# Kernel tuning notes

Hardware: AMD Instinct MI355X
Metric: run time of the kernel (lower is better)

Reference implementation:

```python
import jax, jax.numpy as jnp
import numpy as np

EPS = 1e-5
NHEAD = 8

def layer_norm(x, g, b):
    mu = jnp.mean(x, axis=-1, keepdims=True)
    var = jnp.mean((x - mu) ** 2, axis=-1, keepdims=True)
    return (x - mu) * jax.lax.rsqrt(var + EPS) * g + b

def setup_inputs() -> dict:
    key = jax.random.key(0)
    ks = jax.random.split(key, 8)
    B, S, D, F = 4, 2048, 512, 2048
    s = 0.02
    return {
        "x": jax.random.normal(ks[0], (B, S, D), jnp.float32),
        "Wqkv": jax.random.normal(ks[1], (3 * D, D), jnp.float32) * s,
        "bqkv": jnp.zeros((3 * D,), jnp.float32),
        "Wo": jax.random.normal(ks[2], (D, D), jnp.float32) * s,
        "bo": jnp.zeros((D,), jnp.float32),
        "W1": jax.random.normal(ks[3], (F, D), jnp.float32) * s,
        "b1": jnp.zeros((F,), jnp.float32),
        "W2": jax.random.normal(ks[4], (D, F), jnp.float32) * s,
        "b2": jnp.zeros((D,), jnp.float32),
        "g1": jnp.ones((D,), jnp.float32),
        "bn1": jnp.zeros((D,), jnp.float32),
        "g2": jnp.ones((D,), jnp.float32),
        "bn2": jnp.zeros((D,), jnp.float32),
    }

def reference(x, Wqkv, bqkv, Wo, bo, W1, b1, W2, b2, g1, bn1, g2, bn2):
    B, S, D = x.shape
    H = NHEAD
    hd = D // H
    # fused QKV projection (torch MultiheadAttention in_proj)
    qkv = x @ Wqkv.T + bqkv                      # [B,S,3D]
    q, k, v = jnp.split(qkv, 3, axis=-1)
    q = q.reshape(B, S, H, hd).transpose(0, 2, 1, 3)  # [B,H,S,hd]
    k = k.reshape(B, S, H, hd).transpose(0, 2, 1, 3)
    v = v.reshape(B, S, H, hd).transpose(0, 2, 1, 3)
    scores = jnp.einsum("bhqd,bhkd->bhqk", q, k) / jnp.sqrt(jnp.float32(hd))
    causal = jnp.tril(jnp.ones((S, S), bool))
    scores = jnp.where(causal, scores, jnp.float32(-jnp.inf))
    attn = jax.nn.softmax(scores, axis=-1)
    ctx = jnp.einsum("bhqk,bhkd->bhqd", attn, v)        # [B,H,S,hd]
    ctx = ctx.transpose(0, 2, 1, 3).reshape(B, S, D)
    attn_out = ctx @ Wo.T + bo
    # residual + LayerNorm 1
    x = layer_norm(x + attn_out, g1, bn1)
    # FFN (ReLU) + residual + LayerNorm 2
    ff = jax.nn.relu(x @ W1.T + b1) @ W2.T + b2
    x = layer_norm(x + ff, g2, bn2)
    return x
```

## Files before the change

kernel.cpp:

```cpp
#include <hip/hip_runtime.h>
#include <hip/hip_bf16.h>
#include <math.h>

#define D_MODEL 512
#define SEQ     2048
#define BATCH   4
#define NHEADS  8
#define HDIM    64
#define FFN     2048
#define TOKENS  (BATCH*SEQ)

typedef __attribute__((ext_vector_type(8))) short bf16x8;
typedef __attribute__((ext_vector_type(4))) float f32x4;
typedef __attribute__((ext_vector_type(4))) unsigned u32x4;

__device__ inline ushort f2bf(float f) {
    unsigned u = __builtin_bit_cast(unsigned, f);
    unsigned r = (u + 0x7fffu + ((u >> 16) & 1u)) >> 16;
    return (ushort)r;
}

#define GLOAD_LDS16(g, l) __builtin_amdgcn_global_load_lds( \
    (const __attribute__((address_space(1))) void*)(g), \
    (__attribute__((address_space(3))) void*)(l), 16, 0, 0)

__global__ void cast_all_bf16(const float* __restrict__ x, const float* __restrict__ Wqkv,
                              const float* __restrict__ Wo, const float* __restrict__ W1,
                              const float* __restrict__ W2, ushort* __restrict__ outbase) {
    const int i = blockIdx.x * blockDim.x + threadIdx.x;
    if (i >= 1835008) return;
    float4 v;
    if      (i < 1048576) v = ((const float4*)x)[i];
    else if (i < 1245184) v = ((const float4*)Wqkv)[i - 1048576];
    else if (i < 1310720) v = ((const float4*)Wo)[i - 1245184];
    else if (i < 1572864) v = ((const float4*)W1)[i - 1310720];
    else                  v = ((const float4*)W2)[i - 1572864];
    ushort4 o;
    o.x = f2bf(v.x); o.y = f2bf(v.y); o.z = f2bf(v.z); o.w = f2bf(v.w);
    ((ushort4*)outbase)[i] = o;
}

template<int MODE, int RELU, int BM, int BN>
__global__ __launch_bounds__(BN == 256 ? 512 : 256)
void gemm_bt_mfma(const ushort* __restrict__ A,
                  const ushort* __restrict__ W,
                  const float* __restrict__ bias,
                  void* __restrict__ CoutA,
                  ushort* __restrict__ Qc,
                  ushort* __restrict__ Kc,
                  ushort* __restrict__ Vt,
                  int M, int N, int Kstride, int Klen) {
    constexpr int NW    = (BN == 256) ? 8 : 4;
    constexpr int WC    = NW / 2;
    constexpr int MI    = BM / 32;
    constexpr int AROWS = BM / NW;
    constexpr bool A2   = (AROWS == 32);
    __shared__ ushort Asb[3][BM * 32];
    __shared__ ushort Bsb[3][BN * 32];

    const int tid  = threadIdx.x;
    const int lane = tid & 63;
    const int wv   = tid >> 6;

    const int Gx = gridDim.x;
    const int f  = blockIdx.x + Gx * blockIdx.y;
    const int xc = f & 7;
    const int j  = f >> 3;
    const int ni = j % Gx;
    const int mi = xc * (gridDim.y >> 3) + j / Gx;
    const int m0 = mi * BM;
    const int n0 = ni * BN;

    const int wm = (wv / WC) * (BM / 2);
    const int wn = (wv % WC) * 64;

    const int rA = wv * AROWS + (lane >> 2);
    const int rB = wv * 32 + (lane >> 2);
    const int cS = (((lane & 3) ^ ((lane >> 3) & 3)) * 8);
    const ushort* gA0 = A + (size_t)(m0 + rA) * Kstride + cS;
    const ushort* gA1 = gA0 + (size_t)16 * Kstride;
    const ushort* gB0 = W + (size_t)(n0 + rB) * Kstride + cS;
    const ushort* gB1 = gB0 + (size_t)16 * Kstride;

    f32x4 acc[MI][4] = {};

    const int fr  = lane & 15;
    const int fks = (((lane >> 4) ^ ((fr >> 1) & 3)) * 8);
    const int loA = wv * (AROWS * 32);
    const int loB = wv * 1024;

#define STAGE(ab, bb) do { \
        GLOAD_LDS16(gA0, (ab) + loA); \
        if constexpr (A2) GLOAD_LDS16(gA1, (ab) + loA + 512); \
        GLOAD_LDS16(gB0, (bb) + loB); \
        GLOAD_LDS16(gB1, (bb) + loB + 512); \
        gA0 += 32; if constexpr (A2) gA1 += 32; \
        gB0 += 32; gB1 += 32; } while (0)

#define COMPUTE(ab, bb) do { \
        bf16x8 af_[MI], bf_[4]; \
        _Pragma("unroll") \
        for (int i_ = 0; i_ < MI; ++i_) \
            af_[i_] = *(const bf16x8*)((ab) + (wm + i_ * 16 + fr) * 32 + fks); \
        _Pragma("unroll") \
        for (int j_ = 0; j_ < 4; ++j_) \
            bf_[j_] = *(const bf16x8*)((bb) + (wn + j_ * 16 + fr) * 32 + fks); \
        _Pragma("unroll") \
        for (int i_ = 0; i_ < MI; ++i_) \
            _Pragma("unroll") \
            for (int j_ = 0; j_ < 4; ++j_) \
                acc[i_][j_] = __builtin_amdgcn_mfma_f32_16x16x32_bf16(af_[i_], bf_[j_], acc[i_][j_], 0, 0, 0); \
        } while (0)

#define PWAIT do { \
        if constexpr (A2) asm volatile("s_waitcnt vmcnt(4)" ::: "memory"); \
        else              asm volatile("s_waitcnt vmcnt(3)" ::: "memory"); \
        __builtin_amdgcn_s_barrier(); \
        __builtin_amdgcn_sched_barrier(0); } while (0)

    ushort *Ac = Asb[0], *An = Asb[1], *As = Asb[2];
    ushort *Bc = Bsb[0], *Bn = Bsb[1], *Bs = Bsb[2];

    STAGE(Ac, Bc);
    STAGE(An, Bn);
    const int ntiles = Klen >> 5;
    for (int t = 0; t < ntiles - 1; ++t) {
        PWAIT;
        if (t + 2 < ntiles) STAGE(As, Bs);
        COMPUTE(Ac, Bc);
        ushort* tA = Ac; Ac = An; An = As; As = tA;
        ushort* tB = Bc; Bc = Bn; Bn = Bs; Bs = tB;
    }
    asm volatile("s_waitcnt vmcnt(0)" ::: "memory");
    __builtin_amdgcn_s_barrier();
    __builtin_amdgcn_sched_barrier(0);
    COMPUTE(Ac, Bc);

#undef STAGE
#undef COMPUTE
#undef PWAIT

    const int col  = lane & 15;
    const int rowq = (lane >> 4) * 4;
    #pragma unroll
    for (int i = 0; i < MI; ++i) {
        const int gm = m0 + wm + i * 16 + rowq;
        #pragma unroll
        for (int j2 = 0; j2 < 4; ++j2) {
            const int gn = n0 + wn + j2 * 16 + col;
            if (MODE == 2) {
                const float bv = bias[gn];
                const int seg = gn >> 9;
                const int h   = (gn >> 6) & 7;
                const int dd  = gn & 63;
                const int bb  = gm >> 11;
                const int ss  = gm & 2047;
                const int bh  = bb * 8 + h;
                if (seg == 2) {
                    ushort4 pk;
                    pk.x = f2bf(acc[i][j2][0] + bv);
                    pk.y = f2bf(acc[i][j2][1] + bv);
                    pk.z = f2bf(acc[i][j2][2] + bv);
                    pk.w = f2bf(acc[i][j2][3] + bv);
                    *(ushort4*)(Vt + ((size_t)bh * 64 + dd) * 2048 + ss) = pk;
                } else {
                    ushort* dst = (seg == 0 ? Qc : Kc) + ((size_t)bh * 2048 + ss) * 64 + dd;
                    #pragma unroll
                    for (int r = 0; r < 4; ++r)
                        dst[(size_t)r * 64] = f2bf(acc[i][j2][r] + bv);
                }
            } else if (MODE == 3) {
                float* dst = (float*)CoutA;
                const float bv = bias[gn];
                #pragma unroll
                for (int r = 0; r < 4; ++r)
                    dst[(size_t)(gm + r) * N + gn] = acc[i][j2][r] + bv;
            } else {
                const float bv = bias[gn];
                #pragma unroll
                for (int r = 0; r < 4; ++r) {
                    float v = acc[i][j2][r] + bv;
                    if (RELU) v = fmaxf(v, 0.f);
                    ((ushort*)CoutA)[(size_t)(gm + r) * N + gn] = f2bf(v);
                }
            }
        }
    }
}

__device__ __forceinline__ void attn_step2(const ushort* __restrict__ Kb,
                                           const ushort* __restrict__ Vb,
                                           bf16x8 qfA0, bf16x8 qfA1,
                                           bf16x8 qfB0, bf16x8 qfB1,
                                           float& lpa, float& lpb,
                                           f32x4 (&oa)[4], f32x4 (&ob)[4],
                                           int qwA, int qwB, int j0,
                                           int q0a, int q0b,
                                           int col, int g, int c7) {
    const bool doA = (j0 <= q0a);

    bf16x8 kf0[4], kf1[4];
    #pragma unroll
    for (int nt = 0; nt < 4; ++nt) {
        const int kr = nt * 16 + col;
        kf0[nt] = *(const bf16x8*)(Kb + kr * 64 + (((g    ) ^ c7) * 8));
        kf1[nt] = *(const bf16x8*)(Kb + kr * 64 + (((g + 4) ^ c7) * 8));
    }

    f32x4 sA[4] = {}, sB[4] = {};
    __builtin_amdgcn_s_setprio(1);
    #pragma unroll
    for (int nt = 0; nt < 4; ++nt) {
        sB[nt] = __builtin_amdgcn_mfma_f32_16x16x32_bf16(kf0[nt], qfB0, sB[nt], 0, 0, 0);
        sB[nt] = __builtin_amdgcn_mfma_f32_16x16x32_bf16(kf1[nt], qfB1, sB[nt], 0, 0, 0);
    }
    if (doA) {
        #pragma unroll
        for (int nt = 0; nt < 4; ++nt) {
            sA[nt] = __builtin_amdgcn_mfma_f32_16x16x32_bf16(kf0[nt], qfA0, sA[nt], 0, 0, 0);
            sA[nt] = __builtin_amdgcn_mfma_f32_16x16x32_bf16(kf1[nt], qfA1, sA[nt], 0, 0, 0);
        }
    }
    __builtin_amdgcn_s_setprio(0);

    bf16x8 vf0[4], vf1[4];
    #pragma unroll
    for (int nt = 0; nt < 4; ++nt) {
        const int vr = nt * 16 + col;
        vf0[nt] = *(const bf16x8*)(Vb + vr * 64 + (((g    ) ^ c7) * 8));
        vf1[nt] = *(const bf16x8*)(Vb + vr * 64 + (((g + 4) ^ c7) * 8));
    }

    if (j0 == q0b) {
        #pragma unroll
        for (int nt = 0; nt < 4; ++nt)
            #pragma unroll
            for (int r = 0; r < 4; ++r)
                if ((j0 + nt * 16 + 4 * g + r) > (qwB + col)) sB[nt][r] = -INFINITY;
    }
    unsigned WB[8];
    #pragma unroll
    for (int nt = 0; nt < 4; ++nt) {
        float p0 = __expf(sB[nt][0] * 0.125f);
        float p1 = __expf(sB[nt][1] * 0.125f);
        float p2 = __expf(sB[nt][2] * 0.125f);
        float p3 = __expf(sB[nt][3] * 0.125f);
        lpb += (p0 + p1) + (p2 + p3);
        asm("v_cvt_pk_bf16_f32 %0, %1, %2" : "=v"(WB[2 * nt])     : "v"(p0), "v"(p1));
        asm("v_cvt_pk_bf16_f32 %0, %1, %2" : "=v"(WB[2 * nt + 1]) : "v"(p2), "v"(p3));
    }
    asm("v_permlane32_swap_b32 %0, %1" : "+v"(WB[0]), "+v"(WB[2]));
    asm("v_permlane32_swap_b32 %0, %1" : "+v"(WB[1]), "+v"(WB[3]));
    asm("v_permlane32_swap_b32 %0, %1" : "+v"(WB[4]), "+v"(WB[6]));
    asm("v_permlane32_swap_b32 %0, %1" : "+v"(WB[5]), "+v"(WB[7]));
    asm("v_permlane16_swap_b32 %0, %1" : "+v"(WB[0]), "+v"(WB[2]));
    asm("v_permlane16_swap_b32 %0, %1" : "+v"(WB[1]), "+v"(WB[3]));
    asm("v_permlane16_swap_b32 %0, %1" : "+v"(WB[4]), "+v"(WB[6]));
    asm("v_permlane16_swap_b32 %0, %1" : "+v"(WB[5]), "+v"(WB[7]));
    {
        u32x4 wa = {WB[0], WB[1], WB[2], WB[3]};
        u32x4 wb = {WB[4], WB[5], WB[6], WB[7]};
        bf16x8 pf0 = __builtin_bit_cast(bf16x8, wa);
        bf16x8 pf1 = __builtin_bit_cast(bf16x8, wb);
        __builtin_amdgcn_s_setprio(1);
        #pragma unroll
        for (int nt = 0; nt < 4; ++nt) {
            ob[nt] = __builtin_amdgcn_mfma_f32_16x16x32_bf16(pf0, vf0[nt], ob[nt], 0, 0, 0);
            ob[nt] = __builtin_amdgcn_mfma_f32_16x16x32_bf16(pf1, vf1[nt], ob[nt], 0, 0, 0);
        }
        __builtin_amdgcn_s_setprio(0);
    }

    if (doA) {
        if (j0 == q0a) {
            #pragma unroll
            for (int nt = 0; nt < 4; ++nt)
                #pragma unroll
                for (int r = 0; r < 4; ++r)
                    if ((j0 + nt * 16 + 4 * g + r) > (qwA + col)) sA[nt][r] = -INFINITY;
        }
        unsigned WA[8];
        #pragma unroll
        for (int nt = 0; nt < 4; ++nt) {
            float p0 = __expf(sA[nt][0] * 0.125f);
            float p1 = __expf(sA[nt][1] * 0.125f);
            float p2 = __expf(sA[nt][2] * 0.125f);
            float p3 = __expf(sA[nt][3] * 0.125f);
            lpa += (p0 + p1) + (p2 + p3);
            asm("v_cvt_pk_bf16_f32 %0, %1, %2" : "=v"(WA[2 * nt])     : "v"(p0), "v"(p1));
            asm("v_cvt_pk_bf16_f32 %0, %1, %2" : "=v"(WA[2 * nt + 1]) : "v"(p2), "v"(p3));
        }
        asm("v_permlane32_swap_b32 %0, %1" : "+v"(WA[0]), "+v"(WA[2]));
        asm("v_permlane32_swap_b32 %0, %1" : "+v"(WA[1]), "+v"(WA[3]));
        asm("v_permlane32_swap_b32 %0, %1" : "+v"(WA[4]), "+v"(WA[6]));
        asm("v_permlane32_swap_b32 %0, %1" : "+v"(WA[5]), "+v"(WA[7]));
        asm("v_permlane16_swap_b32 %0, %1" : "+v"(WA[0]), "+v"(WA[2]));
        asm("v_permlane16_swap_b32 %0, %1" : "+v"(WA[1]), "+v"(WA[3]));
        asm("v_permlane16_swap_b32 %0, %1" : "+v"(WA[4]), "+v"(WA[6]));
        asm("v_permlane16_swap_b32 %0, %1" : "+v"(WA[5]), "+v"(WA[7]));
        u32x4 wa = {WA[0], WA[1], WA[2], WA[3]};
        u32x4 wb = {WA[4], WA[5], WA[6], WA[7]};
        bf16x8 pf0 = __builtin_bit_cast(bf16x8, wa);
        bf16x8 pf1 = __builtin_bit_cast(bf16x8, wb);
        __builtin_amdgcn_s_setprio(1);
        #pragma unroll
        for (int nt = 0; nt < 4; ++nt) {
            oa[nt] = __builtin_amdgcn_mfma_f32_16x16x32_bf16(pf0, vf0[nt], oa[nt], 0, 0, 0);
            oa[nt] = __builtin_amdgcn_mfma_f32_16x16x32_bf16(pf1, vf1[nt], oa[nt], 0, 0, 0);
        }
        __builtin_amdgcn_s_setprio(0);
    }
}

__global__ __launch_bounds__(256, 2) void attn_mfma_kernel(const ushort* __restrict__ Qc,
                                                           const ushort* __restrict__ Kc,
                                                           const ushort* __restrict__ Vt,
                                                           ushort* __restrict__ ctxb) {
    __shared__ ushort Ks[2 * 64 * 64];
    __shared__ ushort Vs[2 * 64 * 64];

    const int tid  = threadIdx.x;
    const int lane = tid & 63;
    const int wv   = tid >> 6;
    const int idx  = blockIdx.x;
    const int bh   = (idx & 7) * 4 + (idx >> 7);
    const int pair = (idx >> 3) & 15;
    const int q0a  = pair * 64;
    const int q0b  = (31 - pair) * 64;
    const int qwA  = q0a + wv * 16;
    const int qwB  = q0b + wv * 16;

    const int col = lane & 15;
    const int g   = lane >> 4;
    const int c7  = col & 7;

    bf16x8 qfA0, qfA1, qfB0, qfB1;
    {
        const ushort* qa = Qc + ((size_t)bh * 2048 + qwA + col) * 64 + g * 8;
        qfA0 = *(const bf16x8*)qa;
        qfA1 = *(const bf16x8*)(qa + 32);
        const ushort* qb = Qc + ((size_t)bh * 2048 + qwB + col) * 64 + g * 8;
        qfB0 = *(const bf16x8*)qb;
        qfB1 = *(const bf16x8*)(qb + 32);
    }

    const int l3  = lane >> 3;
    const int swz = ((lane & 7) ^ l3) * 8;
    const ushort* KgL = Kc + ((size_t)bh * 2048 + wv * 8 + l3) * 64 + swz;
    const ushort* VgL = Vt + ((size_t)bh * 64 + wv * 8 + l3) * 2048 + swz;
    const int dW = wv * 512;

#define ASTAGE(par, jj) do { \
        GLOAD_LDS16(KgL + (size_t)(jj) * 64,        Ks + (par) * 4096 + dW); \
        GLOAD_LDS16(KgL + (size_t)(jj) * 64 + 2048, Ks + (par) * 4096 + dW + 2048); \
        GLOAD_LDS16(VgL + (jj),                     Vs + (par) * 4096 + dW); \
        GLOAD_LDS16(VgL + (jj) + 65536,             Vs + (par) * 4096 + dW + 2048); } while (0)

    float lpa = 0.f, lpb = 0.f;
    f32x4 oa[4] = {}, ob[4] = {};

    ASTAGE(0, 0);
    for (int j0 = 0; j0 <= q0b; j0 += 64) {
        const int par = (j0 >> 6) & 1;
        asm volatile("s_waitcnt vmcnt(0)" ::: "memory");
        __builtin_amdgcn_s_barrier();
        __builtin_amdgcn_sched_barrier(0);
        if (j0 < q0b) ASTAGE(par ^ 1, j0 + 64);

        attn_step2(Ks + par * 4096, Vs + par * 4096,
                   qfA0, qfA1, qfB0, qfB1, lpa, lpb, oa, ob,
                   qwA, qwB, j0, q0a, q0b, col, g, c7);
    }
#undef ASTAGE

    float la = lpa; la += __shfl_xor(la, 16); la += __shfl_xor(la, 32);
    float lb = lpb; lb += __shfl_xor(lb, 16); lb += __shfl_xor(lb, 32);
    const int b = bh >> 3, h = bh & 7;
    #pragma unroll
    for (int r = 0; r < 4; ++r) {
        const float inva = 1.f / __shfl(la, 4 * g + r);
        const float invb = 1.f / __shfl(lb, 4 * g + r);
        const size_t rowa = ((size_t)b * 2048 + qwA + 4 * g + r) * 512 + h * 64;
        const size_t rowb = ((size_t)b * 2048 + qwB + 4 * g + r) * 512 + h * 64;
        #pragma unroll
        for (int nt = 0; nt < 4; ++nt) {
            ctxb[rowa + nt * 16 + col] = f2bf(oa[nt][r] * inva);
            ctxb[rowb + nt * 16 + col] = f2bf(ob[nt][r] * invb);
        }
    }
}

template<int WRITE_BF16>
__global__ __launch_bounds__(256) void ln_residual(const float* __restrict__ A,
                            const float* __restrict__ B1,
                            const float* __restrict__ g, const float* __restrict__ beta,
                            float* __restrict__ out, ushort* __restrict__ outb) {
    const int lane = threadIdx.x & 63;
    const int row  = blockIdx.x * 4 + (threadIdx.x >> 6);
    const size_t base = (size_t)row * D_MODEL;
    const int c0 = lane * 4, c1 = 256 + lane * 4;

    float4 a0 = *(const float4*)&A[base + c0];
    float4 a1 = *(const float4*)&A[base + c1];
    float4 b0 = *(const float4*)&B1[base + c0];
    float4 b1 = *(const float4*)&B1[base + c1];
    float v0 = a0.x + b0.x, v1 = a0.y + b0.y, v2 = a0.z + b0.z, v3 = a0.w + b0.w;
    float v4 = a1.x + b1.x, v5 = a1.y + b1.y, v6 = a1.z + b1.z, v7 = a1.w + b1.w;

    float sum = ((v0 + v1) + (v2 + v3)) + ((v4 + v5) + (v6 + v7));
    #pragma unroll
    for (int off = 32; off; off >>= 1) sum += __shfl_xor(sum, off);
    const float mu = sum * (1.f / 512.f);

    float d0 = v0 - mu, d1 = v1 - mu, d2 = v2 - mu, d3 = v3 - mu;
    float d4 = v4 - mu, d5 = v5 - mu, d6 = v6 - mu, d7 = v7 - mu;
    float sq = ((d0 * d0 + d1 * d1) + (d2 * d2 + d3 * d3))
             + ((d4 * d4 + d5 * d5) + (d6 * d6 + d7 * d7));
    #pragma unroll
    for (int off = 32; off; off >>= 1) sq += __shfl_xor(sq, off);
    const float rs = rsqrtf(sq * (1.f / 512.f) + 1e-5f);

    float4 g0 = *(const float4*)&g[c0],    g1 = *(const float4*)&g[c1];
    float4 e0 = *(const float4*)&beta[c0], e1 = *(const float4*)&beta[c1];
    float4 r0, r1;
    r0.x = d0 * rs * g0.x + e0.x; r0.y = d1 * rs * g0.y + e0.y;
    r0.z = d2 * rs * g0.z + e0.z; r0.w = d3 * rs * g0.w + e0.w;
    r1.x = d4 * rs * g1.x + e1.x; r1.y = d5 * rs * g1.y + e1.y;
    r1.z = d6 * rs * g1.z + e1.z; r1.w = d7 * rs * g1.w + e1.w;
    *(float4*)&out[base + c0] = r0;
    *(float4*)&out[base + c1] = r1;
    if (WRITE_BF16) {
        ushort4 u0, u1;
        u0.x = f2bf(r0.x); u0.y = f2bf(r0.y); u0.z = f2bf(r0.z); u0.w = f2bf(r0.w);
        u1.x = f2bf(r1.x); u1.y = f2bf(r1.y); u1.z = f2bf(r1.z); u1.w = f2bf(r1.w);
        *(ushort4*)&outb[base + c0] = u0;
        *(ushort4*)&outb[base + c1] = u1;
    }
}

extern "C" void kernel_launch(void* const* d_in, const int* in_sizes, int n_in,
                              void* d_out, int out_size, void* d_ws, size_t ws_size,
                              hipStream_t stream) {
    const float* x    = (const float*)d_in[0];
    const float* Wqkv = (const float*)d_in[1];
    const float* bqkv = (const float*)d_in[2];
    const float* Wo   = (const float*)d_in[3];
    const float* bo   = (const float*)d_in[4];
    const float* W1   = (const float*)d_in[5];
    const float* b1   = (const float*)d_in[6];
    const float* W2   = (const float*)d_in[7];
    const float* b2   = (const float*)d_in[8];
    const float* g1   = (const float*)d_in[9];
    const float* bn1  = (const float*)d_in[10];
    const float* g2   = (const float*)d_in[11];
    const float* bn2  = (const float*)d_in[12];

    float* ws = (float*)d_ws;
    ushort* Qcb     = (ushort*)ws;
    ushort* Kcb     = (ushort*)(ws + 2097152);
    ushort* Vtb     = (ushort*)(ws + 4194304);
    ushort* ff1b    = (ushort*)ws;
    float*  ff2a    = ws + 8388608;
    float*  attn_a  = ws + 12582912;
    float*  ln1     = ws + 16777216;
    ushort* ctxb  = (ushort*)(ws + 20971520);
    ushort* ln1b  = (ushort*)(ws + 23068672);
    ushort* xb    = (ushort*)(ws + 25165824);
    ushort* Wqkvb = (ushort*)(ws + 27262976);
    float*  out   = (float*)d_out;
    ushort* W1b   = (ushort*)(ws + 27787264);
    ushort* W2b   = (ushort*)(ws + 28311552);
    ushort* Wob   = (ushort*)(ws + 27656192);

    const dim3 blk(256);

    cast_all_bf16<<<dim3(7168), blk, 0, stream>>>(x, Wqkv, Wo, W1, W2, xb);

    gemm_bt_mfma<2,0,128,128><<<dim3(1536/128, 8192/128), blk, 0, stream>>>(
        xb, Wqkvb, bqkv, nullptr, Qcb, Kcb, Vtb, TOKENS, 1536, 512, 512);
    attn_mfma_kernel<<<dim3(512), blk, 0, stream>>>(Qcb, Kcb, Vtb, ctxb);
    gemm_bt_mfma<3,0,64,128><<<dim3(512/128, 8192/64), blk, 0, stream>>>(
        ctxb, Wob, bo, attn_a, nullptr, nullptr, nullptr, TOKENS, 512, 512, 512);
    ln_residual<1><<<dim3(TOKENS/4), blk, 0, stream>>>(x, attn_a, g1, bn1, ln1, ln1b);
    gemm_bt_mfma<1,1,128,256><<<dim3(2048/256, 8192/128), dim3(512), 0, stream>>>(
        ln1b, W1b, b1, ff1b, nullptr, nullptr, nullptr, TOKENS, 2048, 512, 512);
    gemm_bt_mfma<3,0,64,128><<<dim3(512/128, 8192/64), blk, 0, stream>>>(
        ff1b, W2b, b2, ff2a, nullptr, nullptr, nullptr, TOKENS, 512, 2048, 2048);
    ln_residual<0><<<dim3(TOKENS/4), blk, 0, stream>>>(ln1, ff2a, g2, bn2, out, nullptr);
}
```

Before: 242.2 us.

## Load attention K/V fragments directly from global memory instead of LDS staging

Removes the double-buffered LDS staging of K and V tiles, along with its barriers and waitcnt. Each wave now reads its K and V MFMA fragments straight from global memory, with the V loads issued before the QK MFMAs. This drops the LDS footprint and block-wide synchronisation, but each of the four waves now fetches the same K/V data separately, relying on L1/L2 caching and paying global-load latency without explicit prefetch.

```diff
diff --git a/kernel.cpp b/kernel.cpp
--- a/kernel.cpp
+++ b/kernel.cpp
@@ -188,23 +188,29 @@
     }
 }
 
-__device__ __forceinline__ void attn_step2(const ushort* __restrict__ Kb,
-                                           const ushort* __restrict__ Vb,
-                                           bf16x8 qfA0, bf16x8 qfA1,
-                                           bf16x8 qfB0, bf16x8 qfB1,
-                                           float& lpa, float& lpb,
-                                           f32x4 (&oa)[4], f32x4 (&ob)[4],
-                                           int qwA, int qwB, int j0,
-                                           int q0a, int q0b,
-                                           int col, int g, int c7) {
+__device__ __forceinline__ void attn_step2g(const ushort* __restrict__ Kt,
+                                            const ushort* __restrict__ Vg,
+                                            bf16x8 qfA0, bf16x8 qfA1,
+                                            bf16x8 qfB0, bf16x8 qfB1,
+                                            float& lpa, float& lpb,
+                                            f32x4 (&oa)[4], f32x4 (&ob)[4],
+                                            int qwA, int qwB, int j0,
+                                            int q0a, int q0b,
+                                            int col, int g) {
     const bool doA = (j0 <= q0a);
 
-    bf16x8 kf0[4], kf1[4];
+    bf16x8 kf0[4], kf1[4], vf0[4], vf1[4];
     #pragma unroll
     for (int nt = 0; nt < 4; ++nt) {
         const int kr = nt * 16 + col;
-        kf0[nt] = *(const bf16x8*)(Kb + kr * 64 + (((g    ) ^ c7) * 8));
-        kf1[nt] = *(const bf16x8*)(Kb + kr * 64 + (((g + 4) ^ c7) * 8));
+        kf0[nt] = *(const bf16x8*)(Kt + kr * 64 + g * 8);
+        kf1[nt] = *(const bf16x8*)(Kt + kr * 64 + g * 8 + 32);
+    }
+    #pragma unroll
+    for (int nt = 0; nt < 4; ++nt) {
+        const int vr = nt * 16 + col;
+        vf0[nt] = *(const bf16x8*)(Vg + (size_t)vr * 2048 + g * 8);
+        vf1[nt] = *(const bf16x8*)(Vg + (size_t)vr * 2048 + g * 8 + 32);
     }
 
     f32x4 sA[4] = {}, sB[4] = {};
@@ -222,14 +228,6 @@
         }
     }
     __builtin_amdgcn_s_setprio(0);
-
-    bf16x8 vf0[4], vf1[4];
-    #pragma unroll
-    for (int nt = 0; nt < 4; ++nt) {
-        const int vr = nt * 16 + col;
-        vf0[nt] = *(const bf16x8*)(Vb + vr * 64 + (((g    ) ^ c7) * 8));
-        vf1[nt] = *(const bf16x8*)(Vb + vr * 64 + (((g + 4) ^ c7) * 8));
-    }
 
     if (j0 == q0b) {
         #pragma unroll
@@ -316,9 +314,6 @@
                                                            const ushort* __restrict__ Kc,
                                                            const ushort* __restrict__ Vt,
                                                            ushort* __restrict__ ctxb) {
-    __shared__ ushort Ks[2 * 64 * 64];
-    __shared__ ushort Vs[2 * 64 * 64];
-
     const int tid  = threadIdx.x;
     const int lane = tid & 63;
     const int wv   = tid >> 6;
@@ -332,7 +327,6 @@
 
     const int col = lane & 15;
     const int g   = lane >> 4;
-    const int c7  = col & 7;
 
     bf16x8 qfA0, qfA1, qfB0, qfB1;
     {
@@ -344,34 +338,17 @@
         qfB1 = *(const bf16x8*)(qb + 32);
     }
 
-    const int l3  = lane >> 3;
-    const int swz = ((lane & 7) ^ l3) * 8;
-    const ushort* KgL = Kc + ((size_t)bh * 2048 + wv * 8 + l3) * 64 + swz;
-    const ushort* VgL = Vt + ((size_t)bh * 64 + wv * 8 + l3) * 2048 + swz;
-    const int dW = wv * 512;
-
-#define ASTAGE(par, jj) do { \
-        GLOAD_LDS16(KgL + (size_t)(jj) * 64,        Ks + (par) * 4096 + dW); \
-        GLOAD_LDS16(KgL + (size_t)(jj) * 64 + 2048, Ks + (par) * 4096 + dW + 2048); \
-        GLOAD_LDS16(VgL + (jj),                     Vs + (par) * 4096 + dW); \
-        GLOAD_LDS16(VgL + (jj) + 65536,             Vs + (par) * 4096 + dW + 2048); } while (0)
+    const ushort* Kbase = Kc + (size_t)bh * 2048 * 64;
+    const ushort* Vbase = Vt + (size_t)bh * 64 * 2048;
 
     float lpa = 0.f, lpb = 0.f;
     f32x4 oa[4] = {}, ob[4] = {};
 
-    ASTAGE(0, 0);
     for (int j0 = 0; j0 <= q0b; j0 += 64) {
-        const int par = (j0 >> 6) & 1;
-        asm volatile("s_waitcnt vmcnt(0)" ::: "memory");
-        __builtin_amdgcn_s_barrier();
-        __builtin_amdgcn_sched_barrier(0);
-        if (j0 < q0b) ASTAGE(par ^ 1, j0 + 64);
-
-        attn_step2(Ks + par * 4096, Vs + par * 4096,
-                   qfA0, qfA1, qfB0, qfB1, lpa, lpb, oa, ob,
-                   qwA, qwB, j0, q0a, q0b, col, g, c7);
-    }
-#undef ASTAGE
+        attn_step2g(Kbase + (size_t)j0 * 64, Vbase + j0,
+                    qfA0, qfA1, qfB0, qfB1, lpa, lpb, oa, ob,
+                    qwA, qwB, j0, q0a, q0b, col, g);
+    }
 
     float la = lpa; la += __shfl_xor(la, 16); la += __shfl_xor(la, 32);
     float lb = lpb; lb += __shfl_xor(lb, 16); lb += __shfl_xor(lb, 32);
```

New measurement: 321.1 us. 1.33x slower.
